# Kernel tuning notes

Measured on AMD Instinct MI355X. Metric: run time of the kernel, lower is better.

## Reference

```python
import jax, jax.numpy as jnp
import numpy as np

PI = 3.14159265358979323846
MARGIN = 6.0
DIM = 256
ENT_TOT = 43234
REL_RANGE = (6.0 + 2.0) / DIM  # (margin + epsilon) / dim = 0.03125


def setup_inputs() -> dict:
    key = jax.random.key(0)
    k1, k2, k3 = jax.random.split(key, 3)
    head = jax.random.normal(k1, (32, 2 * DIM), dtype=jnp.float32)
    relation = jax.random.normal(k2, (32, DIM), dtype=jnp.float32)
    ent_emb = jax.random.normal(k3, (ENT_TOT, 2 * DIM), dtype=jnp.float32)
    return {"head": head, "relation": relation, "ent_emb": ent_emb}


def reference(head, relation, ent_emb):
    # head: (B, 2D) -> re/im halves (B, D)
    re_h, im_h = jnp.split(head, 2, axis=-1)
    # entity table: (E, 2D) -> (E, D) each
    re_t, im_t = jnp.split(ent_emb, 2, axis=-1)
    # phase rotation from relation embedding
    phase = relation / (REL_RANGE / PI)          # (B, D)
    re_r = jnp.cos(phase)
    im_r = jnp.sin(phase)
    # complex rotation of head by relation: (B, D)
    re_rot = re_h * re_r - im_h * im_r
    im_rot = re_h * im_r + im_h * re_r
    # difference against every entity, broadcast to (B, E, D)
    re_s = re_rot[:, None, :] - re_t[None, :, :]
    im_s = im_rot[:, None, :] - im_t[None, :, :]
    # L2 norm over the complex pair, summed over D -> (B, E)
    dist = jnp.sqrt(re_s * re_s + im_s * im_s).sum(axis=-1)
    return MARGIN - dist
```

## Files before the change

### kernel.cpp

```cpp
#include <hip/hip_runtime.h>
#include <math.h>

#define DIMH 256
#define NB   32
#define E_TOT 43234
#define TE   16
#define DK   16
#define NCW  4

typedef float v2f __attribute__((ext_vector_type(2)));
typedef float v4f __attribute__((ext_vector_type(4)));
typedef __fp16 v2h __attribute__((ext_vector_type(2)));
typedef __fp16 v4h __attribute__((ext_vector_type(4)));

__global__ __launch_bounds__(64) void rot_kernel(const float* __restrict__ head,
                                                 const float* __restrict__ rel,
                                                 float4* __restrict__ rot_v4) {
    int i  = blockIdx.x * 64 + threadIdx.x;
    int b  = i >> 7;
    int dp = i & 127;
    int d0 = dp * 2;
    float4 w;
    {
        float re_h = head[b * 2 * DIMH + d0];
        float im_h = head[b * 2 * DIMH + DIMH + d0];
        float x = rel[b * DIMH + d0] * 16.0f;
        float f = x - floorf(x);
        float s = __builtin_amdgcn_sinf(f);
        float c = __builtin_amdgcn_cosf(f);
        w.x = re_h * c - im_h * s;
        w.y = re_h * s + im_h * c;
    }
    {
        float re_h = head[b * 2 * DIMH + d0 + 1];
        float im_h = head[b * 2 * DIMH + DIMH + d0 + 1];
        float x = rel[b * DIMH + d0 + 1] * 16.0f;
        float f = x - floorf(x);
        float s = __builtin_amdgcn_sinf(f);
        float c = __builtin_amdgcn_cosf(f);
        w.z = re_h * c - im_h * s;
        w.w = re_h * s + im_h * c;
    }
    rot_v4[b * (DIMH / 2) + dp] = w;
}

__device__ __forceinline__ v2h pkrtz(float a, float b) {
    return __builtin_amdgcn_cvt_pkrtz(a, b);
}

#if __has_builtin(__builtin_amdgcn_fdot2)
__device__ __forceinline__ float dot2(v2h a, v2h b, float c) {
    return __builtin_amdgcn_fdot2(a, b, c, false);
}
#else
__device__ __forceinline__ float dot2(v2h a, v2h b, float c) {
    return (float)a.x * (float)b.x + (float)a.y * (float)b.y + c;
}
#endif

__global__ __launch_bounds__(256) void dist_kernel(const float* __restrict__ ent,
                                                   const float4* __restrict__ rot_v4,
                                                   float* __restrict__ out) {
    __shared__ v4h smem[1536];

    const int tid  = threadIdx.x;
    const int lane = tid & 63;
    const int w    = tid >> 6;
    const int eb   = blockIdx.x * TE;
    const int eg   = lane & 7;
    const int bg   = lane >> 3;

    v4h* se = smem + w * 384;
    v4h* sr = se + 128;

    const int erow = lane >> 2;
    const int eq   = lane & 3;
    const int rb   = lane >> 3;
    const int rdpi = lane & 7;

    const int c0 = w * NCW;

    float4 pe_re, pe_im, pr[4];

    auto load_chunk = [&](int c) {
        const int dk = c * DK;
        int er = min(eb + erow, E_TOT - 1);
        const float* b0 = ent + (size_t)er * (2 * DIMH);
        pe_re = *reinterpret_cast<const float4*>(b0 + dk + 4 * eq);
        pe_im = *reinterpret_cast<const float4*>(b0 + DIMH + dk + 4 * eq);
        #pragma unroll
        for (int s = 0; s < 4; ++s)
            pr[s] = rot_v4[(rb + 8 * s) * (DIMH / 2) + c * (DK / 2) + rdpi];
    };

    auto store_chunk = [&]() {
        {
            int row = erow;
            int sw  = (row >> 1) & 7;
            v4h lo, hi;
            lo.xy = pkrtz(pe_re.x, pe_im.x);
            lo.zw = pkrtz(pe_re.y, pe_im.y);
            hi.xy = pkrtz(pe_re.z, pe_im.z);
            hi.zw = pkrtz(pe_re.w, pe_im.w);
            se[row * 8 + ((2 * eq)     ^ sw)] = lo;
            se[row * 8 + ((2 * eq + 1) ^ sw)] = hi;
        }
        #pragma unroll
        for (int s = 0; s < 4; ++s) {
            int b  = rb + 8 * s;
            int sw = (b >> 2) & 7;
            v4h r;
            r.xy = pkrtz(pr[s].x, pr[s].y);
            r.zw = pkrtz(pr[s].z, pr[s].w);
            sr[b * 8 + (rdpi ^ sw)] = r;
        }
    };

    float acc[4][2];
    #pragma unroll
    for (int j = 0; j < 4; ++j)
        #pragma unroll
        for (int k = 0; k < 2; ++k) acc[j][k] = 0.f;

    load_chunk(c0);

    #pragma unroll 1
    for (int cc = 0; cc < NCW; ++cc) {
        store_chunk();
        if (cc + 1 < NCW) load_chunk(c0 + cc + 1);

        #pragma unroll 4
        for (int p = 0; p < DK / 2; ++p) {
            int pe = p ^ eg, pb = p ^ bg;
            v4h r0 = sr[(4 * bg + 0) * 8 + pb];
            v4h r1 = sr[(4 * bg + 1) * 8 + pb];
            v4h r2 = sr[(4 * bg + 2) * 8 + pb];
            v4h r3 = sr[(4 * bg + 3) * 8 + pb];
            v4h e0 = se[(2 * eg + 0) * 8 + pe];
            v4h e1 = se[(2 * eg + 1) * 8 + pe];
            #define CONTRIB(J, K, R, E)                                   \
                { v2h a = R.xy - E.xy;                                    \
                  v2h b = R.zw - E.zw;                                    \
                  float s0 = dot2(a, a, 0.f);                             \
                  float s1 = dot2(b, b, 0.f);                             \
                  acc[J][K] += __builtin_amdgcn_sqrtf(s0)                 \
                             + __builtin_amdgcn_sqrtf(s1); }
            CONTRIB(0,0,r0,e0) CONTRIB(0,1,r0,e1)
            CONTRIB(1,0,r1,e0) CONTRIB(1,1,r1,e1)
            CONTRIB(2,0,r2,e0) CONTRIB(2,1,r2,e1)
            CONTRIB(3,0,r3,e0) CONTRIB(3,1,r3,e1)
            #undef CONTRIB
        }
    }

    float part[8];
    #pragma unroll
    for (int j = 0; j < 4; ++j)
        #pragma unroll
        for (int k = 0; k < 2; ++k)
            part[j * 2 + k] = acc[j][k];

    __syncthreads();
    float* red = (float*)smem;
    #pragma unroll
    for (int i = 0; i < 8; ++i)
        red[tid * 9 + i] = part[i];
    __syncthreads();

    #pragma unroll
    for (int t = 0; t < 2; ++t) {
        int O  = tid + 256 * t;
        int b  = O >> 4;
        int ei = O & 15;
        int e  = eb + ei;
        if (e < E_TOT) {
            int lane_src = ((b >> 2) << 3) + (ei >> 1);
            int idx      = ((b & 3) << 1) + (ei & 1);
            float sum = red[(0 * 64 + lane_src) * 9 + idx]
                      + red[(1 * 64 + lane_src) * 9 + idx]
                      + red[(2 * 64 + lane_src) * 9 + idx]
                      + red[(3 * 64 + lane_src) * 9 + idx];
            out[(size_t)b * E_TOT + e] = 6.0f - sum;
        }
    }
}

extern "C" void kernel_launch(void* const* d_in, const int* in_sizes, int n_in,
                              void* d_out, int out_size, void* d_ws, size_t ws_size,
                              hipStream_t stream) {
    const float* head = (const float*)d_in[0];
    const float* rel  = (const float*)d_in[1];
    const float* ent  = (const float*)d_in[2];
    float4* rot_v4 = (float4*)d_ws;

    rot_kernel<<<(NB * DIMH / 2) / 64, 64, 0, stream>>>(head, rel, rot_v4);

    int etiles = (E_TOT + TE - 1) / TE;
    dist_kernel<<<etiles, 256, 0, stream>>>(ent, rot_v4, (float*)d_out);
}
```

Baseline: 171.1 us.

## Double entity tile per block and widen per-thread register tile to 4x4

Each block now handles 32 entities with 8 waves, and each wave covers two 16-dim chunks instead of four. Each thread accumulates a 4x4 batch-by-entity tile instead of 4x2, so each LDS read of a rotated-head vector is reused across twice as many entities. Staging loads and the swizzle are reorganized to match, and the cross-wave reduction now sums 8 partials. This cuts LDS traffic per FLOP and halves the number of blocks, at the cost of more registers, more LDS per block and a larger reduction.

```diff
diff --git a/kernel.cpp b/kernel.cpp
--- a/kernel.cpp
+++ b/kernel.cpp
@@ -4,9 +4,9 @@
 #define DIMH 256
 #define NB   32
 #define E_TOT 43234
-#define TE   16
+#define TE   32
 #define DK   16
-#define NCW  4
+#define NCW  2
 
 typedef float v2f __attribute__((ext_vector_type(2)));
 typedef float v4f __attribute__((ext_vector_type(4)));
@@ -58,10 +58,10 @@
 }
 #endif
 
-__global__ __launch_bounds__(256) void dist_kernel(const float* __restrict__ ent,
+__global__ __launch_bounds__(512) void dist_kernel(const float* __restrict__ ent,
                                                    const float4* __restrict__ rot_v4,
                                                    float* __restrict__ out) {
-    __shared__ v4h smem[1536];
+    __shared__ v4h smem[4352];
 
     const int tid  = threadIdx.x;
     const int lane = tid & 63;
@@ -70,57 +70,62 @@
     const int eg   = lane & 7;
     const int bg   = lane >> 3;
 
-    v4h* se = smem + w * 384;
-    v4h* sr = se + 128;
-
-    const int erow = lane >> 2;
-    const int eq   = lane & 3;
-    const int rb   = lane >> 3;
-    const int rdpi = lane & 7;
+    v4h* se = smem + w * 512;
+    v4h* sr = se + 256;
+
+    const int srow = lane & 31;
+    const int h    = lane >> 5;
 
     const int c0 = w * NCW;
 
-    float4 pe_re, pe_im, pr[4];
+    float4 pe[4];
+    float4 pr[4];
 
     auto load_chunk = [&](int c) {
         const int dk = c * DK;
-        int er = min(eb + erow, E_TOT - 1);
+        int er = min(eb + srow, E_TOT - 1);
         const float* b0 = ent + (size_t)er * (2 * DIMH);
-        pe_re = *reinterpret_cast<const float4*>(b0 + dk + 4 * eq);
-        pe_im = *reinterpret_cast<const float4*>(b0 + DIMH + dk + 4 * eq);
+        #pragma unroll
+        for (int s = 0; s < 2; ++s) {
+            int q = 2 * h + s;
+            pe[2 * s]     = *reinterpret_cast<const float4*>(b0 + dk + 4 * q);
+            pe[2 * s + 1] = *reinterpret_cast<const float4*>(b0 + DIMH + dk + 4 * q);
+        }
         #pragma unroll
         for (int s = 0; s < 4; ++s)
-            pr[s] = rot_v4[(rb + 8 * s) * (DIMH / 2) + c * (DK / 2) + rdpi];
+            pr[s] = rot_v4[srow * (DIMH / 2) + c * (DK / 2) + 4 * h + s];
     };
 
     auto store_chunk = [&]() {
-        {
-            int row = erow;
-            int sw  = (row >> 1) & 7;
+        const int sw = (srow >> 2) & 7;
+        #pragma unroll
+        for (int s = 0; s < 2; ++s) {
+            int q = 2 * h + s;
             v4h lo, hi;
-            lo.xy = pkrtz(pe_re.x, pe_im.x);
-            lo.zw = pkrtz(pe_re.y, pe_im.y);
-            hi.xy = pkrtz(pe_re.z, pe_im.z);
-            hi.zw = pkrtz(pe_re.w, pe_im.w);
-            se[row * 8 + ((2 * eq)     ^ sw)] = lo;
-            se[row * 8 + ((2 * eq + 1) ^ sw)] = hi;
+            lo.xy = pkrtz(pe[2 * s].x, pe[2 * s + 1].x);
+            lo.zw = pkrtz(pe[2 * s].y, pe[2 * s + 1].y);
+            hi.xy = pkrtz(pe[2 * s].z, pe[2 * s + 1].z);
+            hi.zw = pkrtz(pe[2 * s].w, pe[2 * s + 1].w);
+            se[srow * 8 + ((2 * q)     ^ sw)] = lo;
+            se[srow * 8 + ((2 * q + 1) ^ sw)] = hi;
         }
         #pragma unroll
         for (int s = 0; s < 4; ++s) {
-            int b  = rb + 8 * s;
-            int sw = (b >> 2) & 7;
             v4h r;
             r.xy = pkrtz(pr[s].x, pr[s].y);
             r.zw = pkrtz(pr[s].z, pr[s].w);
-            sr[b * 8 + (rdpi ^ sw)] = r;
+            sr[srow * 8 + ((4 * h + s) ^ sw)] = r;
         }
     };
 
-    float acc[4][2];
+    float acc[4][4];
     #pragma unroll
     for (int j = 0; j < 4; ++j)
         #pragma unroll
-        for (int k = 0; k < 2; ++k) acc[j][k] = 0.f;
+        for (int k = 0; k < 4; ++k) acc[j][k] = 0.f;
+
+    const v4h* sr_b = sr + (4 * bg) * 8;
+    const v4h* se_b = se + (4 * eg) * 8;
 
     load_chunk(c0);
 
@@ -131,13 +136,15 @@
 
         #pragma unroll 4
         for (int p = 0; p < DK / 2; ++p) {
-            int pe = p ^ eg, pb = p ^ bg;
-            v4h r0 = sr[(4 * bg + 0) * 8 + pb];
-            v4h r1 = sr[(4 * bg + 1) * 8 + pb];
-            v4h r2 = sr[(4 * bg + 2) * 8 + pb];
-            v4h r3 = sr[(4 * bg + 3) * 8 + pb];
-            v4h e0 = se[(2 * eg + 0) * 8 + pe];
-            v4h e1 = se[(2 * eg + 1) * 8 + pe];
+            int pb = p ^ bg, pk = p ^ eg;
+            v4h r0 = sr_b[0 * 8 + pb];
+            v4h r1 = sr_b[1 * 8 + pb];
+            v4h r2 = sr_b[2 * 8 + pb];
+            v4h r3 = sr_b[3 * 8 + pb];
+            v4h e0 = se_b[0 * 8 + pk];
+            v4h e1 = se_b[1 * 8 + pk];
+            v4h e2 = se_b[2 * 8 + pk];
+            v4h e3 = se_b[3 * 8 + pk];
             #define CONTRIB(J, K, R, E)                                   \
                 { v2h a = R.xy - E.xy;                                    \
                   v2h b = R.zw - E.zw;                                    \
@@ -145,41 +152,41 @@
                   float s1 = dot2(b, b, 0.f);                             \
                   acc[J][K] += __builtin_amdgcn_sqrtf(s0)                 \
                              + __builtin_amdgcn_sqrtf(s1); }
-            CONTRIB(0,0,r0,e0) CONTRIB(0,1,r0,e1)
-            CONTRIB(1,0,r1,e0) CONTRIB(1,1,r1,e1)
-            CONTRIB(2,0,r2,e0) CONTRIB(2,1,r2,e1)
-            CONTRIB(3,0,r3,e0) CONTRIB(3,1,r3,e1)
+            CONTRIB(0,0,r0,e0) CONTRIB(0,1,r0,e1) CONTRIB(0,2,r0,e2) CONTRIB(0,3,r0,e3)
+            CONTRIB(1,0,r1,e0) CONTRIB(1,1,r1,e1) CONTRIB(1,2,r1,e2) CONTRIB(1,3,r1,e3)
+            CONTRIB(2,0,r2,e0) CONTRIB(2,1,r2,e1) CONTRIB(2,2,r2,e2) CONTRIB(2,3,r2,e3)
+            CONTRIB(3,0,r3,e0) CONTRIB(3,1,r3,e1) CONTRIB(3,2,r3,e2) CONTRIB(3,3,r3,e3)
             #undef CONTRIB
         }
     }
 
-    float part[8];
+    float part[16];
     #pragma unroll
     for (int j = 0; j < 4; ++j)
         #pragma unroll
-        for (int k = 0; k < 2; ++k)
-            part[j * 2 + k] = acc[j][k];
+        for (int k = 0; k < 4; ++k)
+            part[j * 4 + k] = acc[j][k];
 
     __syncthreads();
     float* red = (float*)smem;
     #pragma unroll
-    for (int i = 0; i < 8; ++i)
-        red[tid * 9 + i] = part[i];
+    for (int i = 0; i < 16; ++i)
+        red[tid * 17 + i] = part[i];
     __syncthreads();
 
     #pragma unroll
     for (int t = 0; t < 2; ++t) {
-        int O  = tid + 256 * t;
-        int b  = O >> 4;
-        int ei = O & 15;
+        int O  = tid + 512 * t;
+        int b  = O >> 5;
+        int ei = O & 31;
         int e  = eb + ei;
         if (e < E_TOT) {
-            int lane_src = ((b >> 2) << 3) + (ei >> 1);
-            int idx      = ((b & 3) << 1) + (ei & 1);
-            float sum = red[(0 * 64 + lane_src) * 9 + idx]
-                      + red[(1 * 64 + lane_src) * 9 + idx]
-                      + red[(2 * 64 + lane_src) * 9 + idx]
-                      + red[(3 * 64 + lane_src) * 9 + idx];
+            int lane_src = ((b >> 2) << 3) + (ei >> 2);
+            int idx      = ((b & 3) << 2) + (ei & 3);
+            float sum = 0.f;
+            #pragma unroll
+            for (int w8 = 0; w8 < 8; ++w8)
+                sum += red[(w8 * 64 + lane_src) * 17 + idx];
             out[(size_t)b * E_TOT + e] = 6.0f - sum;
         }
     }
@@ -196,5 +203,5 @@
     rot_kernel<<<(NB * DIMH / 2) / 64, 64, 0, stream>>>(head, rel, rot_v4);
 
     int etiles = (E_TOT + TE - 1) / TE;
-    dist_kernel<<<etiles, 256, 0, stream>>>(ent, rot_v4, (float*)d_out);
-}
+    dist_kernel<<<etiles, 512, 0, stream>>>(ent, rot_v4, (float*)d_out);
+}
```

Measured after the change: 177.6 us. 3.8% more time.
